# Performance work log

Measured on AMD Instinct MI355X. Metric: run time of the kernel, lower is better.

The kernel has to match this reference:

```python
import jax, jax.numpy as jnp
from jax import lax
import numpy as np

B, C, H, W, R = 8, 256, 88, 88, 8
EPS = 1e-5

def _conv(x, w, b, stride=1, pad=0):
    out = lax.conv_general_dilated(x, w, (stride, stride), ((pad, pad), (pad, pad)),
                                   dimension_numbers=('NCHW', 'OIHW', 'NCHW'))
    return out + b[None, :, None, None]

def _bn(x, g, b, m, v):
    # eval-mode BatchNorm2d with running stats
    inv = g * lax.rsqrt(v + EPS)
    return (x - m[None, :, None, None]) * inv[None, :, None, None] + b[None, :, None, None]

def _ln_ch(x, g, b):
    # LayerNorm over the channel dim of an NCHW tensor (torch permutes to NHWC, LN, permute back)
    m = x.mean(axis=1, keepdims=True)
    var = ((x - m) ** 2).mean(axis=1, keepdims=True)
    return (x - m) * lax.rsqrt(var + EPS) * g[None, :, None, None] + b[None, :, None, None]

def _sra(qf, kvf, qw, qb, kw, kb, vw, vb, srw, srb, lng, lnb):
    # SpatialReductionAttention with reduction_ratio R > 1
    Bq, Cq, Hq, Wq = qf.shape
    Q = _conv(qf, qw, qb).reshape(Bq, Cq // 8, Hq * Wq)          # (B, C/8, N)
    kvr = _ln_ch(_conv(kvf, srw, srb, stride=R), lng, lnb)        # (B, C, H/R, W/R)
    K = _conv(kvr, kw, kb).reshape(Bq, Cq // 8, -1)               # (B, C/8, Nr)
    V = _conv(kvr, vw, vb).reshape(Bq, Cq, -1)                    # (B, C, Nr)
    scale = (Cq // 8) ** -0.5
    attn = jax.nn.softmax(jnp.einsum('bcn,bcm->bnm', Q, K) * scale, axis=-1)  # (B, N, Nr)
    return jnp.einsum('bcm,bnm->bcn', V, attn).reshape(Bq, Cq, Hq, Wq)


def setup_inputs() -> dict:
    key = jax.random.key(0)
    ks = iter(jax.random.split(key, 64))
    def nrm(shape, s=0.05):
        return jax.random.normal(next(ks), shape, dtype=jnp.float32) * s
    d = {}
    d['f_rgb'] = nrm((B, C, H, W), 1.0)
    d['f_depth'] = nrm((B, C, H, W), 1.0)
    Ct = 2 * C
    d['sm_w1'] = nrm((Ct // 2, Ct, 3, 3)); d['sm_b1'] = jnp.zeros((Ct // 2,))
    d['sm_g1'] = jnp.ones((Ct // 2,)); d['sm_be1'] = jnp.zeros((Ct // 2,))
    d['sm_m1'] = jnp.zeros((Ct // 2,)); d['sm_v1'] = jnp.ones((Ct // 2,))
    d['sm_w2'] = nrm((1, Ct // 2, 1, 1)); d['sm_b2'] = jnp.zeros((1,))
    for pfx in ('d2r', 'r2d'):
        d[pfx + '_q_w'] = nrm((C // 8, C, 1, 1)); d[pfx + '_q_b'] = jnp.zeros((C // 8,))
        d[pfx + '_k_w'] = nrm((C // 8, C, 1, 1)); d[pfx + '_k_b'] = jnp.zeros((C // 8,))
        d[pfx + '_v_w'] = nrm((C, C, 1, 1)); d[pfx + '_v_b'] = jnp.zeros((C,))
        d[pfx + '_sr_w'] = nrm((C, C, R, R), 0.02); d[pfx + '_sr_b'] = jnp.zeros((C,))
        d[pfx + '_ln_g'] = jnp.ones((C,)); d[pfx + '_ln_b'] = jnp.zeros((C,))
        d[pfx + '_norm_g'] = jnp.ones((C,)); d[pfx + '_norm_b'] = jnp.zeros((C,))
    d['d2r_gamma'] = jnp.full((1,), 0.1, dtype=jnp.float32)
    d['r2d_gamma'] = jnp.full((1,), 0.1, dtype=jnp.float32)
    Cf = 2 * C + 1
    d['fus_w'] = nrm((C, Cf, 3, 3)); d['fus_b'] = jnp.zeros((C,))
    d['fus_g'] = jnp.ones((C,)); d['fus_be'] = jnp.zeros((C,))
    d['fus_m'] = jnp.zeros((C,)); d['fus_v'] = jnp.ones((C,))
    return d


def reference(f_rgb, f_depth,
              sm_w1, sm_b1, sm_g1, sm_be1, sm_m1, sm_v1, sm_w2, sm_b2,
              d2r_q_w, d2r_q_b, d2r_k_w, d2r_k_b, d2r_v_w, d2r_v_b,
              d2r_sr_w, d2r_sr_b, d2r_ln_g, d2r_ln_b, d2r_norm_g, d2r_norm_b,
              r2d_q_w, r2d_q_b, r2d_k_w, r2d_k_b, r2d_v_w, r2d_v_b,
              r2d_sr_w, r2d_sr_b, r2d_ln_g, r2d_ln_b, r2d_norm_g, r2d_norm_b,
              d2r_gamma, r2d_gamma,
              fus_w, fus_b, fus_g, fus_be, fus_m, fus_v):
    # align_depth is Identity (depth_channels == rgb_channels), same spatial size
    concat = jnp.concatenate([f_rgb, f_depth], axis=1)
    h1 = jax.nn.relu(_bn(_conv(concat, sm_w1, sm_b1, pad=1), sm_g1, sm_be1, sm_m1, sm_v1))
    spatial_mask = jax.nn.sigmoid(_conv(h1, sm_w2, sm_b2))            # (B, 1, H, W)
    f_depth_masked = f_depth * spatial_mask

    out_d2r = _sra(f_rgb, f_depth_masked, d2r_q_w, d2r_q_b, d2r_k_w, d2r_k_b,
                   d2r_v_w, d2r_v_b, d2r_sr_w, d2r_sr_b, d2r_ln_g, d2r_ln_b)
    out_d2r = _ln_ch(out_d2r, d2r_norm_g, d2r_norm_b)
    f_rgb_enh = f_rgb + jnp.clip(d2r_gamma, 0.0, 1.0) * out_d2r

    out_r2d = _sra(f_depth_masked, f_rgb, r2d_q_w, r2d_q_b, r2d_k_w, r2d_k_b,
                   r2d_v_w, r2d_v_b, r2d_sr_w, r2d_sr_b, r2d_ln_g, r2d_ln_b)
    out_r2d = _ln_ch(out_r2d, r2d_norm_g, r2d_norm_b)
    f_depth_enh = f_depth + jnp.clip(r2d_gamma, 0.0, 1.0) * out_r2d

    fus_in = jnp.concatenate([f_rgb_enh, f_depth_enh, spatial_mask], axis=1)
    return jax.nn.relu(_bn(_conv(fus_in, fus_w, fus_b, pad=1), fus_g, fus_be, fus_m, fus_v))
```

## Files before the change

### kernel.cpp

```cpp
#include <hip/hip_runtime.h>
#include <hip/hip_bf16.h>


typedef __bf16 bf16x8 __attribute__((ext_vector_type(8)));
typedef float f32x4 __attribute__((ext_vector_type(4)));

#define AS1 __attribute__((address_space(1)))
#define AS3 __attribute__((address_space(3)))
#define DEVI __device__ __forceinline__
#define BARRIER() do { asm volatile("" ::: "memory"); __builtin_amdgcn_s_barrier(); asm volatile("" ::: "memory"); } while (0)

DEVI float bf2f(unsigned short u){
  union { unsigned int i; float f; } v; v.i = ((unsigned int)u) << 16; return v.f;
}
DEVI unsigned short f2bf(float f){
  union { float f; unsigned int i; } v; v.f = f;
  unsigned int x = v.i;
  unsigned int r = (x + 0x7fffu + ((x >> 16) & 1u)) >> 16;
  return (unsigned short)r;
}

__global__ void bnprep_k(const float* __restrict__ g1, const float* __restrict__ be1,
                         const float* __restrict__ m1, const float* __restrict__ v1,
                         const float* __restrict__ b1,
                         const float* __restrict__ gf, const float* __restrict__ bef,
                         const float* __restrict__ mf, const float* __restrict__ vf,
                         const float* __restrict__ bf,
                         float* __restrict__ sc1, float* __restrict__ sh1,
                         float* __restrict__ scf, float* __restrict__ shf)
{
  int c = threadIdx.x;
  float s = g1[c] * rsqrtf(v1[c] + 1e-5f);
  sc1[c] = s; sh1[c] = (b1[c] - m1[c]) * s + be1[c];
  s = gf[c] * rsqrtf(vf[c] + 1e-5f);
  scf[c] = s; shf[c] = (bf[c] - mf[c]) * s + bef[c];
}

__global__ __launch_bounds__(128)
void zero_border_k(unsigned short* __restrict__ buf, int px_el)
{
  int bi = blockIdx.x;
  int img = bi / 356, e = bi - img * 356;
  int y, x;
  if (e < 90){ y = 0; x = e; }
  else if (e < 180){ y = 89; x = e - 90; }
  else if (e < 268){ y = e - 180 + 1; x = 0; }
  else { y = e - 268 + 1; x = 89; }
  size_t pix = ((size_t)img * 90 + y) * 90 + x;
  int t = threadIdx.x;
  if (t < (px_el >> 3))
    *reinterpret_cast<uint4*>(buf + pix * px_el + t * 8) = uint4{0, 0, 0, 0};
}
__global__ __launch_bounds__(256)
void zero_fustail_k(unsigned short* __restrict__ FusPad)
{
  int idx = blockIdx.x * 256 + threadIdx.x;
  int n = idx >> 3, ch = idx & 7;
  int b = n / 7744, s = n - b * 7744;
  int y = s / 88, x = s - y * 88;
  size_t pix = ((size_t)(b * 90 + y + 1)) * 90 + (x + 1);
  *reinterpret_cast<uint4*>(FusPad + pix * 576 + 512 + ch * 8) = uint4{0, 0, 0, 0};
}

__global__ __launch_bounds__(256)
void prep_xpad_k(const float* __restrict__ rgb, const float* __restrict__ dep,
                 unsigned short* __restrict__ Xpad)
{
  __shared__ unsigned short tile[64][65];
  int bi = blockIdx.x;
  int b = bi / 968;
  int rem = bi - b * 968;
  int cblk = rem / 121;
  int pblk = rem - cblk * 121;
  int t = threadIdx.x;
  int pl = t & 63;
  #pragma unroll
  for (int pass = 0; pass < 16; ++pass){
    int cl = pass * 4 + (t >> 6);
    int c = cblk * 64 + cl;
    const float* sp = (c < 256) ? (rgb + ((size_t)b * 256 + c) * 7744)
                                : (dep + ((size_t)b * 256 + (c - 256)) * 7744);
    tile[cl][pl] = f2bf(sp[pblk * 64 + pl]);
  }
  __syncthreads();
  int cl2 = t & 63;
  for (int pass = 0; pass < 16; ++pass){
    int pl2 = pass * 4 + (t >> 6);
    int pixg = pblk * 64 + pl2;
    int y = pixg / 88, x = pixg - y * 88;
    Xpad[(((size_t)b * 90 + y + 1) * 90 + (x + 1)) * 512 + cblk * 64 + cl2] = tile[cl2][pl2];
  }
}

__global__ __launch_bounds__(256)
void prep_w1t_k(const float* __restrict__ w, unsigned short* __restrict__ o)
{
  int co = blockIdx.x, t = threadIdx.x;
  const float* src = w + (size_t)co * 4608 + t * 18;
  unsigned int* op = (unsigned int*)o;
  #pragma unroll
  for (int k = 0; k < 9; ++k){
    unsigned short lo = f2bf(src[k]);
    unsigned short hi = f2bf(src[9 + k]);
    op[((size_t)k * 256 + co) * 256 + t] = lo | ((unsigned int)hi << 16);
  }
}
__global__ __launch_bounds__(256)
void prep_wfus_k(const float* __restrict__ w, unsigned short* __restrict__ o)
{
  int co = blockIdx.x, t = threadIdx.x;
  const float* src = w + (size_t)co * 4617 + t * 18;
  unsigned int* op = (unsigned int*)o;
  #pragma unroll
  for (int k = 0; k < 9; ++k){
    unsigned short lo = f2bf(src[k]);
    unsigned short hi = f2bf(src[9 + k]);
    op[((size_t)k * 256 + co) * 288 + t] = lo | ((unsigned int)hi << 16);
  }
  if (t < 32){
    #pragma unroll
    for (int k = 0; k < 9; ++k){
      unsigned int val = 0;
      if (t == 0) val = (unsigned int)f2bf(w[(size_t)co * 4617 + 512 * 9 + k]);
      op[((size_t)k * 256 + co) * 288 + 256 + t] = val;
    }
  }
}
__global__ __launch_bounds__(256)
void prep_wsr_k(const float* __restrict__ w, unsigned short* __restrict__ o)
{
  __shared__ float ld[64][65];
  int co = blockIdx.x;
  int t = threadIdx.x;
  for (int cib = 0; cib < 256; cib += 64){
    int cil = t >> 2, tq = t & 3;
    const float* src = w + ((size_t)co * 256 + cib + cil) * 64 + tq * 16;
    float v[16];
    #pragma unroll
    for (int k = 0; k < 16; ++k) v[k] = src[k];
    __syncthreads();
    #pragma unroll
    for (int k = 0; k < 16; ++k) ld[cil][tq * 16 + k] = v[k];
    __syncthreads();
    #pragma unroll
    for (int tp = 0; tp < 16; ++tp){
      int tap = tp * 4 + (t >> 6);
      int ci = t & 63;
      o[((size_t)tap * 256 + co) * 256 + cib + ci] = f2bf(ld[ci][tap]);
    }
  }
}
__global__ __launch_bounds__(256)
void tranw_k(const float* __restrict__ in, unsigned short* __restrict__ out, int R, int C)
{
  __shared__ float tl[32][33];
  int tiles_c = C >> 5;
  int tr = (blockIdx.x / tiles_c) << 5, tc = (blockIdx.x % tiles_c) << 5;
  int t = threadIdx.x; int r = t >> 5, c = t & 31;
  #pragma unroll
  for (int p = 0; p < 4; ++p)
    tl[r + p * 8][c] = in[(size_t)(tr + r + p * 8) * C + tc + c];
  __syncthreads();
  #pragma unroll
  for (int p = 0; p < 4; ++p)
    out[(size_t)(tc + r + p * 8) * R + tr + c] = f2bf(tl[c][r + p * 8]);
}
__global__ __launch_bounds__(256)
void wqprep_k(const float* __restrict__ w, unsigned short* __restrict__ o)
{
  int co = blockIdx.x, t = threadIdx.x;
  int c = t >> 3, e = t & 7;
  o[co * 256 + ((c ^ (co & 7)) * 8) + e] = f2bf(w[co * 256 + t]);
}

struct GemmP {
  const unsigned short* A;
  const unsigned short* W;
  const float* ep_scale;
  const float* ep_shift;
  void* out;
  int img_px, row_px, px_el, ch_off, y0, x0;
  int tapw, stridepix, out_w, out_imgpx;
  int Cin, Mtot, Mtiles, Ntiles, k_per;
};

template<int EPI>
__global__ __launch_bounds__(256)
void gemm_k(GemmP p)
{
  __shared__ __bf16 As[2][128 * 64];
  __shared__ __bf16 Bs[2][128 * 64];
  const int t = threadIdx.x;
  const int lane = t & 63;
  const int wid = t >> 6;
  const int wr = wid >> 1, wc = wid & 1;

  const int cpx = gridDim.x >> 3;
  int pid = (blockIdx.x & 7) * cpx + (blockIdx.x >> 3);
  const int mn = p.Mtiles * p.Ntiles;
  int within = pid % mn;
  int slot = pid / mn;
  int mt = within / p.Ntiles;
  int nt = within - mt * p.Ntiles;
  int kb = slot * p.k_per;
  int tap0 = kb / p.Cin;
  int ntap = p.k_per / p.Cin;

  long long apix[4]; int cbg8[4]; int wrow[4];
  #pragma unroll
  for (int i = 0; i < 4; ++i){
    int r = i * 32 + (t >> 3);
    cbg8[i] = ((t & 7) ^ (r & 7)) * 8;
    int n = mt * 128 + r;
    int nc = n < p.Mtot ? n : 0;
    int b = nc / p.out_imgpx; int rr = nc - b * p.out_imgpx;
    int yo = rr / p.out_w;    int xo = rr - yo * p.out_w;
    apix[i] = (long long)b * p.img_px + (long long)(yo * p.stridepix + p.y0) * p.row_px
            + (xo * p.stridepix + p.x0);
    wrow[i] = (nt * 128 + r) * p.Cin + cbg8[i];
  }

  f32x4 acc[4][4];
  #pragma unroll
  for (int i = 0; i < 4; ++i)
    #pragma unroll
    for (int j = 0; j < 4; ++j)
      acc[i][j] = f32x4{0.f, 0.f, 0.f, 0.f};

  const long long wstap = 256LL * p.Cin;

  auto STAGE = [&](int buf, int tap, int cib){
    int dy = tap / p.tapw, dx = tap - dy * p.tapw;
    const unsigned short* wb = p.W + (long long)tap * wstap + cib;
    const long long aoff = (long long)(dy * p.row_px + dx) * p.px_el + p.ch_off + cib;
    #pragma unroll
    for (int i = 0; i < 4; ++i){
      __builtin_amdgcn_global_load_lds(
          (AS1 void*)(p.A + apix[i] * p.px_el + aoff + cbg8[i]),
          (AS3 void*)(&As[buf][i * 2048 + wid * 512]),
          16, 0, 0);
      __builtin_amdgcn_global_load_lds(
          (AS1 void*)(wb + wrow[i]),
          (AS3 void*)(&Bs[buf][i * 2048 + wid * 512]),
          16, 0, 0);
    }
  };

  const int NT = (p.Cin >> 6) * ntap;
  STAGE(0, tap0, 0);
  int tpn = 1, tap_n = tap0 + 1, cib_n = 0;
  int cur = 0;

  for (int kt = 0; kt < NT; ++kt){
    if (kt + 1 < NT){
      STAGE(cur ^ 1, tap_n, cib_n);
      ++tpn; ++tap_n;
      if (tpn == ntap){ tpn = 0; tap_n = tap0; cib_n += 64; }
      asm volatile("s_waitcnt vmcnt(8)" ::: "memory");
    } else {
      asm volatile("s_waitcnt vmcnt(0)" ::: "memory");
    }
    __builtin_amdgcn_s_barrier();
    __builtin_amdgcn_sched_barrier(0);

    #pragma unroll
    for (int ks = 0; ks < 2; ++ks){
      bf16x8 av[4], bv[4];
      #pragma unroll
      for (int mi = 0; mi < 4; ++mi){
        int ar = wr * 64 + mi * 16 + (lane & 15);
        int cb = (ks * 4 + (lane >> 4)) ^ (ar & 7);
        av[mi] = *reinterpret_cast<const bf16x8*>(&As[cur][ar * 64 + cb * 8]);
      }
      #pragma unroll
      for (int ni = 0; ni < 4; ++ni){
        int br = wc * 64 + ni * 16 + (lane & 15);
        int cb = (ks * 4 + (lane >> 4)) ^ (br & 7);
        bv[ni] = *reinterpret_cast<const bf16x8*>(&Bs[cur][br * 64 + cb * 8]);
      }
      #pragma unroll
      for (int mi = 0; mi < 4; ++mi)
        #pragma unroll
        for (int ni = 0; ni < 4; ++ni)
          acc[mi][ni] = __builtin_amdgcn_mfma_f32_16x16x32_bf16(av[mi], bv[ni], acc[mi][ni], 0, 0, 0);
    }

    __builtin_amdgcn_sched_barrier(0);
    __builtin_amdgcn_s_barrier();
    cur ^= 1;
  }

  const int r0 = (lane >> 4) * 4;
  const int c0 = lane & 15;
  #pragma unroll
  for (int mi = 0; mi < 4; ++mi){
    int nbase = mt * 128 + wr * 64 + mi * 16 + r0;
    #pragma unroll
    for (int ni = 0; ni < 4; ++ni){
      int co = nt * 128 + wc * 64 + ni * 16 + c0;
      f32x4 a = acc[mi][ni];
      float* o = (float*)p.out + (size_t)slot * 968 * 256;
      #pragma unroll
      for (int r = 0; r < 4; ++r){
        int n = nbase + r;
        if (n < p.Mtot) o[(size_t)n * 256 + co] = a[r];
      }
    }
  }
}

template<int EPI>
__global__ __launch_bounds__(512, 2)
void gemm256_k(GemmP p)
{
  __shared__ __bf16 As[2][256 * 64];
  __shared__ __bf16 Bs[2][256 * 64];
  const int t = threadIdx.x;
  const int lane = t & 63;
  const int w = t >> 6;
  const int wr = w >> 2, wc = w & 3;
  const int c15 = lane & 15;
  const int h = lane >> 4;

  const int nwg = gridDim.x;
  const int q = nwg >> 3, r8 = nwg & 7;
  const int bid = blockIdx.x;
  const int xcd = bid & 7;
  const int mt = (xcd < r8 ? xcd * (q + 1) : r8 * (q + 1) + (xcd - r8) * q) + (bid >> 3);

  long long apixel[4];
  const unsigned short* wsrc[4];
  int lbase[4];
  #pragma unroll
  for (int i = 0; i < 4; ++i){
    int r = i * 64 + (t >> 3);
    int cb = ((t & 7) ^ (r & 7)) * 8;
    int n = mt * 256 + r;
    int b = n / p.out_imgpx; int rr = n - b * p.out_imgpx;
    int yo = rr / p.out_w;   int xo = rr - yo * p.out_w;
    long long pix = (long long)b * p.img_px + (long long)(yo * p.stridepix + p.y0) * p.row_px
                  + (xo * p.stridepix + p.x0);
    apixel[i] = pix * p.px_el + p.ch_off + cb;
    wsrc[i] = p.W + (long long)r * p.Cin + cb;
    lbase[i] = i * 4096 + w * 512;
  }

  f32x4 acc[8][4];
  #pragma unroll
  for (int i = 0; i < 8; ++i)
    #pragma unroll
    for (int j = 0; j < 4; ++j)
      acc[i][j] = f32x4{0.f, 0.f, 0.f, 0.f};

  const long long wstap = 256LL * p.Cin;
  const int ntap = p.k_per / p.Cin;
  const int NT = (p.Cin >> 6) * ntap;

  auto STG = [&](int buf, int i, long long aoff, long long woff){
    __builtin_amdgcn_global_load_lds(
        (AS1 void*)(p.A + apixel[i] + aoff),
        (AS3 void*)(&As[buf][lbase[i]]), 16, 0, 0);
    __builtin_amdgcn_global_load_lds(
        (AS1 void*)(wsrc[i] + woff),
        (AS3 void*)(&Bs[buf][lbase[i]]), 16, 0, 0);
  };
  auto LDA = [&](bf16x8* av, int mi0, int ks, int buf){
    #pragma unroll
    for (int m = 0; m < 4; ++m){
      int ar = wr * 128 + (mi0 + m) * 16 + c15;
      int cb = (ks * 4 + h) ^ (ar & 7);
      av[m] = *reinterpret_cast<const bf16x8*>(&As[buf][ar * 64 + cb * 8]);
    }
  };
  auto LDB = [&](bf16x8* bv, int ks, int buf){
    #pragma unroll
    for (int n = 0; n < 4; ++n){
      int br = wc * 64 + n * 16 + c15;
      int cb = (ks * 4 + h) ^ (br & 7);
      bv[n] = *reinterpret_cast<const bf16x8*>(&Bs[buf][br * 64 + cb * 8]);
    }
  };
  auto MM = [&](bf16x8* av, bf16x8* bv, int mi0){
    __builtin_amdgcn_s_setprio(1);
    #pragma unroll
    for (int m = 0; m < 4; ++m)
      #pragma unroll
      for (int n = 0; n < 4; ++n)
        acc[mi0 + m][n] = __builtin_amdgcn_mfma_f32_16x16x32_bf16(av[m], bv[n], acc[mi0 + m][n], 0, 0, 0);
    __builtin_amdgcn_s_setprio(0);
  };

  #pragma unroll
  for (int i = 0; i < 4; ++i) STG(0, i, 0, 0);

  int tap_n = 1, cib_n = 0;
  int cur = 0;

  for (int kt = 0; kt < NT; ++kt){
    const bool last = (kt == NT - 1);
    long long aoff_n = 0, woff_n = 0;
    if (!last){
      int dy = tap_n / p.tapw, dx = tap_n - dy * p.tapw;
      aoff_n = (long long)(dy * p.row_px + dx) * p.px_el + cib_n;
      woff_n = (long long)tap_n * wstap + cib_n;
    }
    bf16x8 av[4], bv[4];

    if (!last){
      STG(cur ^ 1, 0, aoff_n, woff_n);
      asm volatile("s_waitcnt vmcnt(2)" ::: "memory");
    } else {
      asm volatile("s_waitcnt vmcnt(0)" ::: "memory");
    }
    BARRIER();
    LDA(av, 0, 0, cur); LDB(bv, 0, cur);
    MM(av, bv, 0);
    BARRIER();
    LDA(av, 4, 0, cur);
    if (!last) STG(cur ^ 1, 1, aoff_n, woff_n);
    BARRIER();
    MM(av, bv, 4);
    BARRIER();
    LDA(av, 0, 1, cur); LDB(bv, 1, cur);
    if (!last) STG(cur ^ 1, 2, aoff_n, woff_n);
    BARRIER();
    MM(av, bv, 0);
    BARRIER();
    LDA(av, 4, 1, cur);
    if (!last) STG(cur ^ 1, 3, aoff_n, woff_n);
    BARRIER();
    MM(av, bv, 4);
    BARRIER();

    cur ^= 1;
    if (!last){ ++tap_n; if (tap_n == ntap){ tap_n = 0; cib_n += 64; } }
  }

  const int r0 = (lane >> 4) * 4;
  #pragma unroll
  for (int mi = 0; mi < 8; ++mi){
    int nbase = mt * 256 + wr * 128 + mi * 16 + r0;
    #pragma unroll
    for (int ni = 0; ni < 4; ++ni){
      int co = wc * 64 + ni * 16 + c15;
      f32x4 a = acc[mi][ni];
      if constexpr (EPI == 0){
        float sc = p.ep_scale[co], sh = p.ep_shift[co];
        unsigned short* o = (unsigned short*)p.out;
        #pragma unroll
        for (int r = 0; r < 4; ++r){
          float v = fmaf(a[r], sc, sh); v = v > 0.f ? v : 0.f;
          o[(size_t)(nbase + r) * 256 + co] = f2bf(v);
        }
      } else {
        float sc = p.ep_scale[co], sh = p.ep_shift[co];
        float* o = (float*)p.out;
        int b = nbase / 7744; int s = nbase - b * 7744;
        float4 v;
        v.x = fmaxf(fmaf(a[0], sc, sh), 0.f);
        v.y = fmaxf(fmaf(a[1], sc, sh), 0.f);
        v.z = fmaxf(fmaf(a[2], sc, sh), 0.f);
        v.w = fmaxf(fmaf(a[3], sc, sh), 0.f);
        *reinterpret_cast<float4*>(o + ((size_t)(b * 256 + co)) * 7744 + s) = v;
      }
    }
  }
}

__global__ __launch_bounds__(256)
void mask_k(const unsigned short* __restrict__ h1, const float* __restrict__ w2,
            const float* __restrict__ b2, float* __restrict__ mask,
            unsigned short* __restrict__ FusPad)
{
  __shared__ float w[256];
  int t = threadIdx.x;
  w[t] = w2[t];
  __syncthreads();
  int n = blockIdx.x * 256 + t;
  const unsigned short* row = h1 + (size_t)n * 256;
  float s = b2[0];
  for (int c = 0; c < 256; c += 8){
    union { uint4 v; unsigned short s_[8]; } u;
    u.v = *reinterpret_cast<const uint4*>(row + c);
    #pragma unroll
    for (int j = 0; j < 8; ++j) s = fmaf(bf2f(u.s_[j]), w[c + j], s);
  }
  float m = 1.f / (1.f + __expf(-s));
  mask[n] = m;
  int b = n / 7744, sr = n - b * 7744;
  int y = sr / 88, x = sr - y * 88;
  FusPad[(((size_t)b * 90 + y + 1) * 90 + (x + 1)) * 576 + 512] = f2bf(m);
}

__global__ __launch_bounds__(256)
void fdm_k(const unsigned short* __restrict__ Xpad, const float* __restrict__ mask,
           unsigned short* __restrict__ fdm)
{
  int idx = blockIdx.x * 256 + threadIdx.x;
  int n = idx >> 5, cb = idx & 31;
  int b = n / 7744, s = n - b * 7744;
  int y = s / 88, x = s - y * 88;
  size_t pix = ((size_t)(b * 90 + y + 1)) * 90 + x + 1;
  union { uint4 v; unsigned short s_[8]; } u, w;
  u.v = *reinterpret_cast<const uint4*>(Xpad + pix * 512 + 256 + cb * 8);
  float m = mask[n];
  #pragma unroll
  for (int j = 0; j < 8; ++j) w.s_[j] = f2bf(bf2f(u.s_[j]) * m);
  *reinterpret_cast<uint4*>(fdm + (size_t)n * 256 + cb * 8) = w.v;
}

__global__ __launch_bounds__(256)
void lnkvr_k(const float* __restrict__ part, const float* __restrict__ srb,
             const float* __restrict__ lng, const float* __restrict__ lnb,
             unsigned short* __restrict__ kvr)
{
  int n = blockIdx.x, t = threadIdx.x;
  float v = srb[t];
  for (int s = 0; s < 16; ++s) v += part[((size_t)s * 968 + n) * 256 + t];
  float s1 = v, s2 = v * v;
  #pragma unroll
  for (int o = 1; o < 64; o <<= 1){ s1 += __shfl_xor(s1, o, 64); s2 += __shfl_xor(s2, o, 64); }
  __shared__ float a1[4], a2[4];
  if ((t & 63) == 0){ a1[t >> 6] = s1; a2[t >> 6] = s2; }
  __syncthreads();
  float t1 = a1[0] + a1[1] + a1[2] + a1[3];
  float t2 = a2[0] + a2[1] + a2[2] + a2[3];
  float mean = t1 * (1.f / 256.f);
  float var = t2 * (1.f / 256.f) - mean * mean;
  float rstd = rsqrtf(var + 1e-5f);
  kvr[(size_t)n * 256 + t] = f2bf((v - mean) * rstd * lng[t] + lnb[t]);
}

__global__ __launch_bounds__(256)
void dotconv_k(const unsigned short* __restrict__ src,
               const unsigned short* __restrict__ wt, const float* __restrict__ bias,
               float* __restrict__ out)
{
  __shared__ unsigned short wl[256 * 32];
  const int t = threadIdx.x;
  {
    uint4* d = (uint4*)wl; const uint4* s = (const uint4*)wt;
    #pragma unroll
    for (int k = 0; k < 4; ++k) d[t + 256 * k] = s[t + 256 * k];
  }
  __syncthreads();
  const int n = blockIdx.x * 8 + (t >> 5);
  const int co = t & 31;
  const unsigned short* row = src + (size_t)n * 256;
  float sum = bias[co];
  for (int c = 0; c < 256; c += 8){
    union { uint4 v; unsigned short s_[8]; } u;
    u.v = *reinterpret_cast<const uint4*>(row + c);
    #pragma unroll
    for (int j = 0; j < 8; ++j)
      sum = fmaf(bf2f(u.s_[j]), bf2f(wl[(c + j) * 32 + co]), sum);
  }
  out[(size_t)n * 32 + co] = sum;
}

__global__ __launch_bounds__(256)
void vconv_k(const unsigned short* __restrict__ kvr, const unsigned short* __restrict__ vwt,
             const float* __restrict__ vb, unsigned short* __restrict__ VBt)
{
  __shared__ float rowf[256];
  const int n = blockIdx.x, t = threadIdx.x;
  rowf[t] = bf2f(kvr[(size_t)n * 256 + t]);
  __syncthreads();
  float sum = vb[t];
  #pragma unroll 8
  for (int c = 0; c < 256; ++c)
    sum = fmaf(rowf[c], bf2f(vwt[(size_t)c * 256 + t]), sum);
  int b = n / 121, m = n - b * 121;
  VBt[(size_t)b * 32768 + (size_t)t * 128 + m] = f2bf(sum);
}

__global__ __launch_bounds__(512, 2)
void attn_k(const unsigned short* __restrict__ Qsrc, int qmode,
            const unsigned short* __restrict__ wq, const float* __restrict__ qb,
            const float* __restrict__ Kbuf,
            const unsigned short* __restrict__ VBt,
            const unsigned short* __restrict__ Xpad, int resChOff,
            unsigned short* __restrict__ FusPad, int outChOff,
            const float* __restrict__ ng, const float* __restrict__ nbv,
            const float* __restrict__ gammap)
{
  __shared__ unsigned short Vt[2][256][64];
  __shared__ unsigned short Pl[2][128][64];
  __shared__ unsigned short Qs[128][64];
  __shared__ unsigned short Ks[128][64];
  __shared__ unsigned short Wqs[32][256];

  const int t = threadIdx.x;
  const int lane = t & 63;
  const int w = t >> 6;
  const int c15 = lane & 15;
  const int h = lane >> 4;

  const int bid = blockIdx.x;
  const int b = bid / 61;
  const int rb = bid - b * 61;
  const int nb0 = rb * 128;

  const unsigned short* vsrc = VBt + (size_t)b * 32768;
  #pragma unroll
  for (int kt = 0; kt < 2; ++kt)
    #pragma unroll
    for (int i = 0; i < 4; ++i){
      int rowbase = i * 64 + w * 8;
      int c = rowbase + (lane >> 3);
      int mchunk = (lane & 7) ^ (c & 7);
      __builtin_amdgcn_global_load_lds(
        (AS1 void*)(vsrc + (size_t)c * 128 + kt * 64 + mchunk * 8),
        (AS3 void*)(&Vt[kt][rowbase][0]),
        16, 0, 0);
    }

  {
    uint4* d = (uint4*)&Wqs[0][0]; const uint4* s = (const uint4*)wq;
    d[t] = s[t];
    d[t + 512] = s[t + 512];
  }
  {
    int m = t >> 2, part = t & 3;
    union { uint4 v; unsigned short s_[8]; } u;
    u.v = uint4{0, 0, 0, 0};
    if (m < 121){
      const float* kp = Kbuf + ((size_t)b * 121 + m) * 32 + part * 8;
      float4 a = *reinterpret_cast<const float4*>(kp);
      float4 bb = *reinterpret_cast<const float4*>(kp + 4);
      u.s_[0] = f2bf(a.x); u.s_[1] = f2bf(a.y); u.s_[2] = f2bf(a.z); u.s_[3] = f2bf(a.w);
      u.s_[4] = f2bf(bb.x); u.s_[5] = f2bf(bb.y); u.s_[6] = f2bf(bb.z); u.s_[7] = f2bf(bb.w);
    }
    *reinterpret_cast<uint4*>(&Ks[m][(part ^ (m & 7)) * 8]) = u.v;
  }
  __syncthreads();

  const int nA = w * 16 + c15;
  const float scale = 0.17677669529663687f;

  {
    int gn = nb0 + nA; if (gn > 7743) gn = 7743;
    const unsigned short* xrow;
    if (qmode){
      int y = gn / 88, x = gn - y * 88;
      xrow = Qsrc + (((size_t)(b * 90) + y + 1) * 90 + (x + 1)) * 512;
    } else {
      xrow = Qsrc + ((size_t)b * 7744 + gn) * 256;
    }
    f32x4 qacc[2];
    qacc[0] = f32x4{0.f, 0.f, 0.f, 0.f};
    qacc[1] = f32x4{0.f, 0.f, 0.f, 0.f};
    #pragma unroll
    for (int kt = 0; kt < 8; ++kt){
      bf16x8 ax = *reinterpret_cast<const bf16x8*>(xrow + kt * 32 + h * 8);
      #pragma unroll
      for (int ni = 0; ni < 2; ++ni){
        int co = ni * 16 + c15;
        bf16x8 bw = *reinterpret_cast<const bf16x8*>(&Wqs[co][((kt * 4 + h) ^ (co & 7)) * 8]);
        qacc[ni] = __builtin_amdgcn_mfma_f32_16x16x32_bf16(ax, bw, qacc[ni], 0, 0, 0);
      }
    }
    #pragma unroll
    for (int ni = 0; ni < 2; ++ni){
      int co = ni * 16 + c15;
      float bq = qb[co];
      #pragma unroll
      for (int r = 0; r < 4; ++r){
        int n = w * 16 + 4 * h + r;
        int chunk = (co >> 3) ^ (n & 7);
        Qs[n][chunk * 8 + (co & 7)] = f2bf((qacc[ni][r] + bq) * scale);
      }
    }
  }

  bf16x8 aq = *reinterpret_cast<const bf16x8*>(&Qs[nA][(h ^ (nA & 7)) * 8]);
  f32x4 sv[8];
  #pragma unroll
  for (int ni = 0; ni < 8; ++ni){
    int mrow = ni * 16 + c15;
    bf16x8 bk = *reinterpret_cast<const bf16x8*>(&Ks[mrow][(h ^ (mrow & 7)) * 8]);
    sv[ni] = __builtin_amdgcn_mfma_f32_16x16x32_bf16(aq, bk, f32x4{0.f,0.f,0.f,0.f}, 0, 0, 0);
  }
  if (c15 >= 9) sv[7] = f32x4{-1e30f, -1e30f, -1e30f, -1e30f};

  float rden[4];
  #pragma unroll
  for (int r = 0; r < 4; ++r){
    float mx = sv[0][r];
    #pragma unroll
    for (int ni = 1; ni < 8; ++ni) mx = fmaxf(mx, sv[ni][r]);
    #pragma unroll
    for (int o = 1; o < 16; o <<= 1) mx = fmaxf(mx, __shfl_xor(mx, o, 64));
    float sm = 0.f;
    #pragma unroll
    for (int ni = 0; ni < 8; ++ni){
      float p = __expf(sv[ni][r] - mx);
      sv[ni][r] = p;
      sm += p;
    }
    #pragma unroll
    for (int o = 1; o < 16; o <<= 1) sm += __shfl_xor(sm, o, 64);
    rden[r] = 1.f / sm;
  }
  #pragma unroll
  for (int ni = 0; ni < 8; ++ni){
    int m = ni * 16 + c15;
    int kt = m >> 6;
    int mq = (m & 63) >> 3;
    #pragma unroll
    for (int r = 0; r < 4; ++r){
      int n = w * 16 + 4 * h + r;
      Pl[kt][n][(mq ^ (n & 7)) * 8 + (m & 7)] = f2bf(sv[ni][r] * rden[r]);
    }
  }

  bf16x8 pa[2][2];
  #pragma unroll
  for (int kt = 0; kt < 2; ++kt)
    #pragma unroll
    for (int ks = 0; ks < 2; ++ks)
      pa[kt][ks] = *reinterpret_cast<const bf16x8*>(&Pl[kt][nA][((ks * 4 + h) ^ (nA & 7)) * 8]);

  f32x4 acc[16];
  #pragma unroll
  for (int ni = 0; ni < 16; ++ni) acc[ni] = f32x4{0.f, 0.f, 0.f, 0.f};
  #pragma unroll
  for (int ni = 0; ni < 16; ++ni){
    int crow = ni * 16 + c15;
    #pragma unroll
    for (int kt = 0; kt < 2; ++kt)
      #pragma unroll
      for (int ks = 0; ks < 2; ++ks){
        bf16x8 bv = *reinterpret_cast<const bf16x8*>(&Vt[kt][crow][((ks * 4 + h) ^ (crow & 7)) * 8]);
        acc[ni] = __builtin_amdgcn_mfma_f32_16x16x32_bf16(pa[kt][ks], bv, acc[ni], 0, 0, 0);
      }
  }

  float ngv[16], nbb[16];
  #pragma unroll
  for (int ni = 0; ni < 16; ++ni){
    int c = ni * 16 + c15;
    ngv[ni] = ng[c]; nbb[ni] = nbv[c];
  }
  float g = gammap[0]; g = fminf(fmaxf(g, 0.f), 1.f);

  #pragma unroll
  for (int r = 0; r < 4; ++r){
    float s1 = 0.f, s2 = 0.f;
    #pragma unroll
    for (int ni = 0; ni < 16; ++ni){ float v = acc[ni][r]; s1 += v; s2 += v * v; }
    #pragma unroll
    for (int o = 1; o < 16; o <<= 1){ s1 += __shfl_xor(s1, o, 64); s2 += __shfl_xor(s2, o, 64); }
    float mean = s1 * (1.f / 256.f);
    float var = s2 * (1.f / 256.f) - mean * mean;
    float rstd = rsqrtf(var + 1e-5f);

    int nloc = w * 16 + 4 * h + r;
    int rix = nb0 + nloc;
    if (rix < 7744){
      int y = rix / 88, x = rix - y * 88;
      size_t pix = ((size_t)(b * 90) + y + 1) * 90 + (x + 1);
      const unsigned short* res = Xpad + pix * 512 + resChOff;
      unsigned short* outp = FusPad + pix * 576 + outChOff;
      #pragma unroll
      for (int ni = 0; ni < 16; ++ni){
        int c = ni * 16 + c15;
        float yv = (acc[ni][r] - mean) * rstd * ngv[ni] + nbb[ni];
        outp[c] = f2bf(bf2f(res[c]) + g * yv);
      }
    }
  }
}

extern "C" void kernel_launch(void* const* d_in, const int* in_sizes, int n_in,
                              void* d_out, int out_size, void* d_ws, size_t ws_size,
                              hipStream_t stream)
{
  const float* P[42];
  for (int i = 0; i < 42; ++i) P[i] = (const float*)d_in[i];

  char* ws = (char*)d_ws;
  size_t off = 0;
  auto take = [&](size_t bytes) -> char* {
    char* p = ws + off; off += (bytes + 255) & ~(size_t)255; return p;
  };
  unsigned short* XPAD = (unsigned short*)take(8ull * 8100 * 512 * 2);
  unsigned short* FUSP = (unsigned short*)take(8ull * 8100 * 576 * 2);
  unsigned short* H1   = (unsigned short*)take(61952ull * 256 * 2);
  unsigned short* FDM  = H1;
  unsigned short* W1T  = (unsigned short*)take(9ull * 256 * 512 * 2);
  unsigned short* WFT  = (unsigned short*)take(9ull * 256 * 576 * 2);
  unsigned short* WSRA = (unsigned short*)take(64ull * 256 * 256 * 2);
  unsigned short* WSRB = (unsigned short*)take(64ull * 256 * 256 * 2);
  float* PART = (float*)take(16ull * 968 * 256 * 4);
  unsigned short* KVR = (unsigned short*)take(968ull * 256 * 2);
  float* KB   = (float*)take(968ull * 32 * 4);
  unsigned short* VBT = (unsigned short*)take(8ull * 256 * 128 * 2);
  float* MASK = (float*)take(61952ull * 4);
  float* SC1 = (float*)take(256 * 4);
  float* SH1 = (float*)take(256 * 4);
  float* SCF = (float*)take(256 * 4);
  float* SHF = (float*)take(256 * 4);
  unsigned short* WQSA = (unsigned short*)take(32ull * 256 * 2);
  unsigned short* WQSB = (unsigned short*)take(32ull * 256 * 2);
  unsigned short* KWTA = (unsigned short*)take(256ull * 32 * 2);
  unsigned short* VWTA = (unsigned short*)take(256ull * 256 * 2);
  unsigned short* KWTB = (unsigned short*)take(256ull * 32 * 2);
  unsigned short* VWTB = (unsigned short*)take(256ull * 256 * 2);
  (void)ws_size; (void)in_sizes; (void)n_in; (void)out_size;

  zero_border_k<<<8 * 356, 128, 0, stream>>>(XPAD, 512);
  zero_border_k<<<8 * 356, 128, 0, stream>>>(FUSP, 576);
  zero_fustail_k<<<1936, 256, 0, stream>>>(FUSP);
  hipMemsetAsync(VBT, 0, 8ull * 256 * 128 * 2, stream);

  bnprep_k<<<1, 256, 0, stream>>>(P[4], P[5], P[6], P[7], P[3],
                                  P[38], P[39], P[40], P[41], P[37],
                                  SC1, SH1, SCF, SHF);
  prep_xpad_k<<<7744, 256, 0, stream>>>(P[0], P[1], XPAD);
  prep_w1t_k<<<256, 256, 0, stream>>>(P[2], W1T);
  prep_wfus_k<<<256, 256, 0, stream>>>(P[36], WFT);
  prep_wsr_k<<<256, 256, 0, stream>>>(P[16], WSRA);
  prep_wsr_k<<<256, 256, 0, stream>>>(P[28], WSRB);
  wqprep_k<<<32, 256, 0, stream>>>(P[10], WQSA);
  wqprep_k<<<32, 256, 0, stream>>>(P[22], WQSB);
  tranw_k<<<8, 256, 0, stream>>>(P[12], KWTA, 32, 256);
  tranw_k<<<64, 256, 0, stream>>>(P[14], VWTA, 256, 256);
  tranw_k<<<8, 256, 0, stream>>>(P[24], KWTB, 32, 256);
  tranw_k<<<64, 256, 0, stream>>>(P[26], VWTB, 256, 256);

  GemmP g1{};
  g1.A = XPAD; g1.W = W1T; g1.ep_scale = SC1; g1.ep_shift = SH1; g1.out = H1;
  g1.img_px = 8100; g1.row_px = 90; g1.px_el = 512; g1.ch_off = 0; g1.y0 = 0; g1.x0 = 0;
  g1.tapw = 3; g1.stridepix = 1; g1.out_w = 88; g1.out_imgpx = 7744;
  g1.Cin = 512; g1.Mtot = 61952; g1.Mtiles = 242; g1.Ntiles = 1; g1.k_per = 4608;
  gemm256_k<0><<<242, 512, 0, stream>>>(g1);

  mask_k<<<242, 256, 0, stream>>>(H1, P[8], P[9], MASK, FUSP);
  fdm_k<<<7744, 256, 0, stream>>>(XPAD, MASK, FDM);

  GemmP gs{};
  gs.A = FDM; gs.W = WSRA; gs.out = PART;
  gs.img_px = 7744; gs.row_px = 88; gs.px_el = 256; gs.ch_off = 0; gs.y0 = 0; gs.x0 = 0;
  gs.tapw = 8; gs.stridepix = 8; gs.out_w = 11; gs.out_imgpx = 121;
  gs.Cin = 256; gs.Mtot = 968; gs.Mtiles = 8; gs.Ntiles = 2; gs.k_per = 1024;
  gemm_k<2><<<256, 256, 0, stream>>>(gs);
  lnkvr_k<<<968, 256, 0, stream>>>(PART, P[17], P[18], P[19], KVR);
  dotconv_k<<<121, 256, 0, stream>>>(KVR, KWTA, P[13], KB);
  vconv_k<<<968, 256, 0, stream>>>(KVR, VWTA, P[15], VBT);
  attn_k<<<488, 512, 0, stream>>>(XPAD, 1, WQSA, P[11], KB, VBT, XPAD, 0,
                                  FUSP, 0, P[20], P[21], P[34]);

  gs.A = XPAD; gs.W = WSRB;
  gs.img_px = 8100; gs.row_px = 90; gs.px_el = 512; gs.y0 = 1; gs.x0 = 1;
  gemm_k<2><<<256, 256, 0, stream>>>(gs);
  lnkvr_k<<<968, 256, 0, stream>>>(PART, P[29], P[30], P[31], KVR);
  dotconv_k<<<121, 256, 0, stream>>>(KVR, KWTB, P[25], KB);
  vconv_k<<<968, 256, 0, stream>>>(KVR, VWTB, P[27], VBT);
  attn_k<<<488, 512, 0, stream>>>(FDM, 0, WQSB, P[23], KB, VBT, XPAD, 256,
                                  FUSP, 256, P[32], P[33], P[35]);

  GemmP gf{};
  gf.A = FUSP; gf.W = WFT; gf.ep_scale = SCF; gf.ep_shift = SHF; gf.out = d_out;
  gf.img_px = 8100; gf.row_px = 90; gf.px_el = 576; gf.ch_off = 0; gf.y0 = 0; gf.x0 = 0;
  gf.tapw = 3; gf.stridepix = 1; gf.out_w = 88; gf.out_imgpx = 7744;
  gf.Cin = 576; gf.Mtot = 61952; gf.Mtiles = 242; gf.Ntiles = 1; gf.k_per = 5184;
  gemm256_k<1><<<242, 512, 0, stream>>>(gf);
}
```

Measured before the change: 552.6 us.

## Batch both attention branches into single launches and deepen gemm256 prefetch

The two spatial-reduction attention branches (d2r and r2d) now run together in shared launches: one SR-conv GEMM covers both sides with half the split-K slots each, one layernorm kernel, one fused V/K projection kernel, and one attention kernel with 976 blocks. This cuts the number of launches and fills more of the GPU at once instead of running two half-sized passes back to back. Separately, the main 3x3 conv GEMM issues two global-to-shared stage loads up front and keeps separate A/B register fragments, so memory latency overlaps more with MFMA work at the cost of more registers. The K projection now runs on only 32 threads per block inside the V kernel, which may be slow.

```diff
diff --git a/kernel.cpp b/kernel.cpp
--- a/kernel.cpp
+++ b/kernel.cpp
@@ -184,12 +184,9 @@
   int Cin, Mtot, Mtiles, Ntiles, k_per;
 };
 
-template<int EPI>
-__global__ __launch_bounds__(256)
-void gemm_k(GemmP p)
-{
-  __shared__ __bf16 As[2][128 * 64];
-  __shared__ __bf16 Bs[2][128 * 64];
+__global__ __launch_bounds__(256)
+void gemm_sr_k(GemmP pa, GemmP pb, float* __restrict__ outA, float* __restrict__ outB)
+{
   const int t = threadIdx.x;
   const int lane = t & 63;
   const int wid = t >> 6;
@@ -197,6 +194,14 @@
 
   const int cpx = gridDim.x >> 3;
   int pid = (blockIdx.x & 7) * cpx + (blockIdx.x >> 3);
+  const int side = pid >= 128;
+  const GemmP& p = side ? pb : pa;
+  float* outp = side ? outB : outA;
+  pid &= 127;
+
+  __shared__ __bf16 As[2][128 * 64];
+  __shared__ __bf16 Bs[2][128 * 64];
+
   const int mn = p.Mtiles * p.Ntiles;
   int within = pid % mn;
   int slot = pid / mn;
@@ -299,7 +304,7 @@
     for (int ni = 0; ni < 4; ++ni){
       int co = nt * 128 + wc * 64 + ni * 16 + c0;
       f32x4 a = acc[mi][ni];
-      float* o = (float*)p.out + (size_t)slot * 968 * 256;
+      float* o = outp + (size_t)slot * 968 * 256;
       #pragma unroll
       for (int r = 0; r < 4; ++r){
         int n = nbase + r;
@@ -395,6 +400,7 @@
 
   int tap_n = 1, cib_n = 0;
   int cur = 0;
+  bf16x8 A0[4], A1[4], B0[4], B1[4];
 
   for (int kt = 0; kt < NT; ++kt){
     const bool last = (kt == NT - 1);
@@ -404,32 +410,31 @@
       aoff_n = (long long)(dy * p.row_px + dx) * p.px_el + cib_n;
       woff_n = (long long)tap_n * wstap + cib_n;
     }
-    bf16x8 av[4], bv[4];
 
     if (!last){
       STG(cur ^ 1, 0, aoff_n, woff_n);
-      asm volatile("s_waitcnt vmcnt(2)" ::: "memory");
+      STG(cur ^ 1, 1, aoff_n, woff_n);
+      asm volatile("s_waitcnt vmcnt(4)" ::: "memory");
     } else {
       asm volatile("s_waitcnt vmcnt(0)" ::: "memory");
     }
     BARRIER();
-    LDA(av, 0, 0, cur); LDB(bv, 0, cur);
-    MM(av, bv, 0);
+    LDA(A0, 0, 0, cur); LDB(B0, 0, cur);
+    MM(A0, B0, 0);
     BARRIER();
-    LDA(av, 4, 0, cur);
-    if (!last) STG(cur ^ 1, 1, aoff_n, woff_n);
-    BARRIER();
-    MM(av, bv, 4);
-    BARRIER();
-    LDA(av, 0, 1, cur); LDB(bv, 1, cur);
+    LDA(A1, 4, 0, cur);
     if (!last) STG(cur ^ 1, 2, aoff_n, woff_n);
     BARRIER();
-    MM(av, bv, 0);
+    MM(A1, B0, 4);
     BARRIER();
-    LDA(av, 4, 1, cur);
+    LDA(A0, 0, 1, cur); LDB(B1, 1, cur);
     if (!last) STG(cur ^ 1, 3, aoff_n, woff_n);
     BARRIER();
-    MM(av, bv, 4);
+    MM(A0, B1, 0);
+    BARRIER();
+    LDA(A1, 4, 1, cur);
+    BARRIER();
+    MM(A1, B1, 4);
     BARRIER();
 
     cur ^= 1;
@@ -510,13 +515,22 @@
 }
 
 __global__ __launch_bounds__(256)
-void lnkvr_k(const float* __restrict__ part, const float* __restrict__ srb,
-             const float* __restrict__ lng, const float* __restrict__ lnb,
-             unsigned short* __restrict__ kvr)
+void lnkvr2_k(const float* __restrict__ partA, const float* __restrict__ partB,
+              const float* __restrict__ srbA, const float* __restrict__ srbB,
+              const float* __restrict__ lngA, const float* __restrict__ lngB,
+              const float* __restrict__ lnbA, const float* __restrict__ lnbB,
+              unsigned short* __restrict__ kvrA, unsigned short* __restrict__ kvrB)
 {
   int n = blockIdx.x, t = threadIdx.x;
+  int side = n >= 968; n -= side * 968;
+  const float* part = side ? partB : partA;
+  const float* srb = side ? srbB : srbA;
+  const float* lng = side ? lngB : lngA;
+  const float* lnb = side ? lnbB : lnbA;
+  unsigned short* kvr = side ? kvrB : kvrA;
+
   float v = srb[t];
-  for (int s = 0; s < 16; ++s) v += part[((size_t)s * 968 + n) * 256 + t];
+  for (int s = 0; s < 8; ++s) v += part[((size_t)s * 968 + n) * 256 + t];
   float s1 = v, s2 = v * v;
   #pragma unroll
   for (int o = 1; o < 64; o <<= 1){ s1 += __shfl_xor(s1, o, 64); s2 += __shfl_xor(s2, o, 64); }
@@ -532,38 +546,26 @@
 }
 
 __global__ __launch_bounds__(256)
-void dotconv_k(const unsigned short* __restrict__ src,
-               const unsigned short* __restrict__ wt, const float* __restrict__ bias,
-               float* __restrict__ out)
-{
-  __shared__ unsigned short wl[256 * 32];
+void vconv2_k(const unsigned short* __restrict__ kvrA, const unsigned short* __restrict__ kvrB,
+              const unsigned short* __restrict__ vwtA, const unsigned short* __restrict__ vwtB,
+              const float* __restrict__ vbA, const float* __restrict__ vbB,
+              const unsigned short* __restrict__ kwtA, const unsigned short* __restrict__ kwtB,
+              const float* __restrict__ kbA, const float* __restrict__ kbB,
+              unsigned short* __restrict__ VBtA, unsigned short* __restrict__ VBtB,
+              float* __restrict__ KBA, float* __restrict__ KBB)
+{
+  int n = blockIdx.x;
+  int side = n >= 968; n -= side * 968;
+  const unsigned short* kvr = side ? kvrB : kvrA;
+  const unsigned short* vwt = side ? vwtB : vwtA;
+  const float* vb = side ? vbB : vbA;
+  const unsigned short* kwt = side ? kwtB : kwtA;
+  const float* kbias = side ? kbB : kbA;
+  unsigned short* VBt = side ? VBtB : VBtA;
+  float* KB = side ? KBB : KBA;
+
+  __shared__ float rowf[256];
   const int t = threadIdx.x;
-  {
-    uint4* d = (uint4*)wl; const uint4* s = (const uint4*)wt;
-    #pragma unroll
-    for (int k = 0; k < 4; ++k) d[t + 256 * k] = s[t + 256 * k];
-  }
-  __syncthreads();
-  const int n = blockIdx.x * 8 + (t >> 5);
-  const int co = t & 31;
-  const unsigned short* row = src + (size_t)n * 256;
-  float sum = bias[co];
-  for (int c = 0; c < 256; c += 8){
-    union { uint4 v; unsigned short s_[8]; } u;
-    u.v = *reinterpret_cast<const uint4*>(row + c);
-    #pragma unroll
-    for (int j = 0; j < 8; ++j)
-      sum = fmaf(bf2f(u.s_[j]), bf2f(wl[(c + j) * 32 + co]), sum);
-  }
-  out[(size_t)n * 32 + co] = sum;
-}
-
-__global__ __launch_bounds__(256)
-void vconv_k(const unsigned short* __restrict__ kvr, const unsigned short* __restrict__ vwt,
-             const float* __restrict__ vb, unsigned short* __restrict__ VBt)
-{
-  __shared__ float rowf[256];
-  const int n = blockIdx.x, t = threadIdx.x;
   rowf[t] = bf2f(kvr[(size_t)n * 256 + t]);
   __syncthreads();
   float sum = vb[t];
@@ -572,17 +574,32 @@
     sum = fmaf(rowf[c], bf2f(vwt[(size_t)c * 256 + t]), sum);
   int b = n / 121, m = n - b * 121;
   VBt[(size_t)b * 32768 + (size_t)t * 128 + m] = f2bf(sum);
-}
+
+  if (t < 32){
+    float ks = kbias[t];
+    #pragma unroll 8
+    for (int c = 0; c < 256; ++c)
+      ks = fmaf(rowf[c], bf2f(kwt[c * 32 + t]), ks);
+    KB[(size_t)n * 32 + t] = ks;
+  }
+}
+
+struct AttnS {
+  const unsigned short* Qsrc;
+  const unsigned short* wq;
+  const float* qb;
+  const float* Kbuf;
+  const unsigned short* VBt;
+  const float* ng;
+  const float* nb;
+  const float* gm;
+  int qmode, resOff, outOff;
+};
 
 __global__ __launch_bounds__(512, 2)
-void attn_k(const unsigned short* __restrict__ Qsrc, int qmode,
-            const unsigned short* __restrict__ wq, const float* __restrict__ qb,
-            const float* __restrict__ Kbuf,
-            const unsigned short* __restrict__ VBt,
-            const unsigned short* __restrict__ Xpad, int resChOff,
-            unsigned short* __restrict__ FusPad, int outChOff,
-            const float* __restrict__ ng, const float* __restrict__ nbv,
-            const float* __restrict__ gammap)
+void attn2_k(AttnS s0, AttnS s1,
+             const unsigned short* __restrict__ Xpad,
+             unsigned short* __restrict__ FusPad)
 {
   __shared__ unsigned short Vt[2][256][64];
   __shared__ unsigned short Pl[2][128][64];
@@ -590,18 +607,22 @@
   __shared__ unsigned short Ks[128][64];
   __shared__ unsigned short Wqs[32][256];
 
+  int bid = blockIdx.x;
+  const int side = bid >= 488;
+  bid -= side * 488;
+  const AttnS& s = side ? s1 : s0;
+
   const int t = threadIdx.x;
   const int lane = t & 63;
   const int w = t >> 6;
   const int c15 = lane & 15;
   const int h = lane >> 4;
 
-  const int bid = blockIdx.x;
   const int b = bid / 61;
   const int rb = bid - b * 61;
   const int nb0 = rb * 128;
 
-  const unsigned short* vsrc = VBt + (size_t)b * 32768;
+  const unsigned short* vsrc = s.VBt + (size_t)b * 32768;
   #pragma unroll
   for (int kt = 0; kt < 2; ++kt)
     #pragma unroll
@@ -616,16 +637,16 @@
     }
 
   {
-    uint4* d = (uint4*)&Wqs[0][0]; const uint4* s = (const uint4*)wq;
-    d[t] = s[t];
-    d[t + 512] = s[t + 512];
+    uint4* d = (uint4*)&Wqs[0][0]; const uint4* sw = (const uint4*)s.wq;
+    d[t] = sw[t];
+    d[t + 512] = sw[t + 512];
   }
   {
     int m = t >> 2, part = t & 3;
     union { uint4 v; unsigned short s_[8]; } u;
     u.v = uint4{0, 0, 0, 0};
     if (m < 121){
-      const float* kp = Kbuf + ((size_t)b * 121 + m) * 32 + part * 8;
+      const float* kp = s.Kbuf + ((size_t)b * 121 + m) * 32 + part * 8;
       float4 a = *reinterpret_cast<const float4*>(kp);
       float4 bb = *reinterpret_cast<const float4*>(kp + 4);
       u.s_[0] = f2bf(a.x); u.s_[1] = f2bf(a.y); u.s_[2] = f2bf(a.z); u.s_[3] = f2bf(a.w);
@@ -641,11 +662,11 @@
   {
     int gn = nb0 + nA; if (gn > 7743) gn = 7743;
     const unsigned short* xrow;
-    if (qmode){
+    if (s.qmode){
       int y = gn / 88, x = gn - y * 88;
-      xrow = Qsrc + (((size_t)(b * 90) + y + 1) * 90 + (x + 1)) * 512;
+      xrow = s.Qsrc + (((size_t)(b * 90) + y + 1) * 90 + (x + 1)) * 512;
     } else {
-      xrow = Qsrc + ((size_t)b * 7744 + gn) * 256;
+      xrow = s.Qsrc + ((size_t)b * 7744 + gn) * 256;
     }
     f32x4 qacc[2];
     qacc[0] = f32x4{0.f, 0.f, 0.f, 0.f};
@@ -663,7 +684,7 @@
     #pragma unroll
     for (int ni = 0; ni < 2; ++ni){
       int co = ni * 16 + c15;
-      float bq = qb[co];
+      float bq = s.qb[co];
       #pragma unroll
       for (int r = 0; r < 4; ++r){
         int n = w * 16 + 4 * h + r;
@@ -740,9 +761,9 @@
   #pragma unroll
   for (int ni = 0; ni < 16; ++ni){
     int c = ni * 16 + c15;
-    ngv[ni] = ng[c]; nbb[ni] = nbv[c];
-  }
-  float g = gammap[0]; g = fminf(fmaxf(g, 0.f), 1.f);
+    ngv[ni] = s.ng[c]; nbb[ni] = s.nb[c];
+  }
+  float g = s.gm[0]; g = fminf(fmaxf(g, 0.f), 1.f);
 
   #pragma unroll
   for (int r = 0; r < 4; ++r){
@@ -760,8 +781,8 @@
     if (rix < 7744){
       int y = rix / 88, x = rix - y * 88;
       size_t pix = ((size_t)(b * 90) + y + 1) * 90 + (x + 1);
-      const unsigned short* res = Xpad + pix * 512 + resChOff;
-      unsigned short* outp = FusPad + pix * 576 + outChOff;
+      const unsigned short* res = Xpad + pix * 512 + s.resOff;
+      unsigned short* outp = FusPad + pix * 576 + s.outOff;
       #pragma unroll
       for (int ni = 0; ni < 16; ++ni){
         int c = ni * 16 + c15;
@@ -792,10 +813,14 @@
   unsigned short* WFT  = (unsigned short*)take(9ull * 256 * 576 * 2);
   unsigned short* WSRA = (unsigned short*)take(64ull * 256 * 256 * 2);
   unsigned short* WSRB = (unsigned short*)take(64ull * 256 * 256 * 2);
-  float* PART = (float*)take(16ull * 968 * 256 * 4);
-  unsigned short* KVR = (unsigned short*)take(968ull * 256 * 2);
-  float* KB   = (float*)take(968ull * 32 * 4);
-  unsigned short* VBT = (unsigned short*)take(8ull * 256 * 128 * 2);
+  float* PARTA = (float*)take(8ull * 968 * 256 * 4);
+  float* PARTB = (float*)take(8ull * 968 * 256 * 4);
+  unsigned short* KVRA = (unsigned short*)take(968ull * 256 * 2);
+  unsigned short* KVRB = (unsigned short*)take(968ull * 256 * 2);
+  float* KBA  = (float*)take(968ull * 32 * 4);
+  float* KBB  = (float*)take(968ull * 32 * 4);
+  unsigned short* VBTA = (unsigned short*)take(2ull * 8 * 256 * 128 * 2);
+  unsigned short* VBTB = VBTA + 8ull * 256 * 128;
   float* MASK = (float*)take(61952ull * 4);
   float* SC1 = (float*)take(256 * 4);
   float* SH1 = (float*)take(256 * 4);
@@ -812,7 +837,7 @@
   zero_border_k<<<8 * 356, 128, 0, stream>>>(XPAD, 512);
   zero_border_k<<<8 * 356, 128, 0, stream>>>(FUSP, 576);
   zero_fustail_k<<<1936, 256, 0, stream>>>(FUSP);
-  hipMemsetAsync(VBT, 0, 8ull * 256 * 128 * 2, stream);
+  hipMemsetAsync(VBTA, 0, 2ull * 8 * 256 * 128 * 2, stream);
 
   bnprep_k<<<1, 256, 0, stream>>>(P[4], P[5], P[6], P[7], P[3],
                                   P[38], P[39], P[40], P[41], P[37],
@@ -839,26 +864,25 @@
   mask_k<<<242, 256, 0, stream>>>(H1, P[8], P[9], MASK, FUSP);
   fdm_k<<<7744, 256, 0, stream>>>(XPAD, MASK, FDM);
 
-  GemmP gs{};
-  gs.A = FDM; gs.W = WSRA; gs.out = PART;
-  gs.img_px = 7744; gs.row_px = 88; gs.px_el = 256; gs.ch_off = 0; gs.y0 = 0; gs.x0 = 0;
-  gs.tapw = 8; gs.stridepix = 8; gs.out_w = 11; gs.out_imgpx = 121;
-  gs.Cin = 256; gs.Mtot = 968; gs.Mtiles = 8; gs.Ntiles = 2; gs.k_per = 1024;
-  gemm_k<2><<<256, 256, 0, stream>>>(gs);
-  lnkvr_k<<<968, 256, 0, stream>>>(PART, P[17], P[18], P[19], KVR);
-  dotconv_k<<<121, 256, 0, stream>>>(KVR, KWTA, P[13], KB);
-  vconv_k<<<968, 256, 0, stream>>>(KVR, VWTA, P[15], VBT);
-  attn_k<<<488, 512, 0, stream>>>(XPAD, 1, WQSA, P[11], KB, VBT, XPAD, 0,
-                                  FUSP, 0, P[20], P[21], P[34]);
-
-  gs.A = XPAD; gs.W = WSRB;
-  gs.img_px = 8100; gs.row_px = 90; gs.px_el = 512; gs.y0 = 1; gs.x0 = 1;
-  gemm_k<2><<<256, 256, 0, stream>>>(gs);
-  lnkvr_k<<<968, 256, 0, stream>>>(PART, P[29], P[30], P[31], KVR);
-  dotconv_k<<<121, 256, 0, stream>>>(KVR, KWTB, P[25], KB);
-  vconv_k<<<968, 256, 0, stream>>>(KVR, VWTB, P[27], VBT);
-  attn_k<<<488, 512, 0, stream>>>(FDM, 0, WQSB, P[23], KB, VBT, XPAD, 256,
-                                  FUSP, 256, P[32], P[33], P[35]);
+  GemmP ga{};
+  ga.A = FDM; ga.W = WSRA; ga.out = nullptr;
+  ga.img_px = 7744; ga.row_px = 88; ga.px_el = 256; ga.ch_off = 0; ga.y0 = 0; ga.x0 = 0;
+  ga.tapw = 8; ga.stridepix = 8; ga.out_w = 11; ga.out_imgpx = 121;
+  ga.Cin = 256; ga.Mtot = 968; ga.Mtiles = 8; ga.Ntiles = 2; ga.k_per = 2048;
+  GemmP gb = ga;
+  gb.A = XPAD; gb.W = WSRB;
+  gb.img_px = 8100; gb.row_px = 90; gb.px_el = 512; gb.y0 = 1; gb.x0 = 1;
+  gemm_sr_k<<<256, 256, 0, stream>>>(ga, gb, PARTA, PARTB);
+
+  lnkvr2_k<<<1936, 256, 0, stream>>>(PARTA, PARTB, P[17], P[29], P[18], P[30],
+                                     P[19], P[31], KVRA, KVRB);
+  vconv2_k<<<1936, 256, 0, stream>>>(KVRA, KVRB, VWTA, VWTB, P[15], P[27],
+                                     KWTA, KWTB, P[13], P[25],
+                                     VBTA, VBTB, KBA, KBB);
+
+  AttnS s0{XPAD, WQSA, P[11], KBA, VBTA, P[20], P[21], P[34], 1, 0, 0};
+  AttnS s1{FDM,  WQSB, P[23], KBB, VBTB, P[32], P[33], P[35], 0, 256, 256};
+  attn2_k<<<976, 512, 0, stream>>>(s0, s1, XPAD, FUSP);
 
   GemmP gf{};
   gf.A = FUSP; gf.W = WFT; gf.ep_scale = SCF; gf.ep_shift = SHF; gf.out = d_out;
```

After: 547.3 us. About the same (-1.0%).
